# Kernel tuning notes

Measured on AMD Instinct MI355X. Metric: run time of the kernel, lower is better.

Reference implementation:

```python
import jax, jax.numpy as jnp
import numpy as np

ALPHA = 0.2  # LeakyReLU negative slope
MASK_VAL = -9e15


def setup_inputs() -> dict:
    key = jax.random.key(0)
    k1, k2, k3, k4 = jax.random.split(key, 4)
    B, N, F_IN = 4, 2048, 256
    H, HD = 8, 32  # out_features = H*HD = 256
    x = jax.random.normal(k1, (B, N, F_IN), dtype=jnp.float32)
    adj = jax.random.randint(k2, (B, N, N), 0, 2, dtype=jnp.int32)
    W = jax.random.normal(k3, (H, F_IN, HD), dtype=jnp.float32) * (1.0 / np.sqrt(F_IN))
    a = jax.random.normal(k4, (H, 2 * HD, 1), dtype=jnp.float32) * 0.1
    return {"x": x, "adj": adj, "W": W, "a": a}


def reference(x, adj, W, a):
    # x: (B,N,F), W: (H,F,D), a: (H,2D,1)
    B, N, _ = x.shape
    H, _, D = W.shape
    Wh = jnp.einsum('bnf,hfd->bhnd', x, W)  # (B,H,N,D)
    # Split additive attention vector: cat([Wh_i, Wh_j]) @ a == Wh_i@a1 + Wh_j@a2
    a1 = a[:, :D, 0]   # (H,D)
    a2 = a[:, D:, 0]   # (H,D)
    s1 = jnp.einsum('bhnd,hd->bhn', Wh, a1)  # source scores
    s2 = jnp.einsum('bhnd,hd->bhn', Wh, a2)  # target scores
    e = jax.nn.leaky_relu(s1[:, :, :, None] + s2[:, :, None, :], negative_slope=ALPHA)  # (B,H,N,N)
    e = jnp.where(adj[:, None, :, :] == 0, MASK_VAL, e)
    attention = jax.nn.softmax(e, axis=-1)  # dropout skipped (eval mode)
    h = jnp.einsum('bhij,bhjd->bhid', attention, Wh)  # (B,H,N,D)
    h = jnp.transpose(h, (0, 2, 1, 3)).reshape(B, N, H * D)
    return jax.nn.elu(h)
```

## Files before the change

kernel.cpp:

```cpp
#include <hip/hip_runtime.h>
#include <hip/hip_bf16.h>

#define ALPHA 0.2f

typedef __attribute__((ext_vector_type(8))) short short8;
typedef __attribute__((ext_vector_type(4))) short s4;
typedef __attribute__((ext_vector_type(8))) _Float16 h8;
typedef __attribute__((ext_vector_type(2))) _Float16 h2v;
typedef __attribute__((ext_vector_type(4))) float f32x4;
typedef __attribute__((ext_vector_type(2))) short sh2;

static constexpr int B = 4, N = 2048, F = 256, H = 8, D = 32;
static constexpr int SZ_X = B * N * F, SZ_ADJ = B * N * N, SZ_W = H * F * D, SZ_A = H * 2 * D;
static const float C1 = 1.4426950408889634f;
static const float C2 = ALPHA * 1.4426950408889634f;


__device__ __forceinline__ unsigned rne16(unsigned u) {
    return u + 0x7fffu + ((u >> 16) & 1u);
}
__device__ __forceinline__ unsigned pk_rne(float a, float b) {
    return __builtin_amdgcn_perm(rne16(__float_as_uint(b)),
                                 rne16(__float_as_uint(a)), 0x07060302u);
}
__device__ __forceinline__ unsigned h2mul(unsigned a, unsigned b) {
    h2v r = __builtin_bit_cast(h2v, a) * __builtin_bit_cast(h2v, b);
    return __builtin_bit_cast(unsigned, r);
}
__device__ __forceinline__ unsigned h2max(unsigned a, unsigned b) {
    h2v r = __builtin_elementwise_max(__builtin_bit_cast(h2v, a),
                                      __builtin_bit_cast(h2v, b));
    return __builtin_bit_cast(unsigned, r);
}
__device__ __forceinline__ unsigned dup16f(float x) {
    unsigned short w = __builtin_bit_cast(unsigned short, (_Float16)x);
    return (unsigned)w | ((unsigned)w << 16);
}
__device__ __forceinline__ unsigned bits2mask(unsigned mk, unsigned mulc) {
    unsigned w = (mk & 3u) * mulc;
    sh2 s = __builtin_bit_cast(sh2, w);
    s = s >> 15;
    return __builtin_bit_cast(unsigned, s);
}

__global__ void k0_prep(const float* __restrict__ Wp, const float* __restrict__ ap,
                        unsigned short* __restrict__ WT2, float* __restrict__ AF) {
    int bid = blockIdx.x;
    int h = bid >> 5, d = bid & 31;
    int f = threadIdx.x;
    unsigned short v = (unsigned short)(rne16(__float_as_uint(Wp[(h * F + f) * D + d])) >> 16);
    WT2[(size_t)(f >> 5) * 8192 + (h * 32 + d) * 32 + (f & 31)] = v;
    if (d == 0 && f < 64) AF[h * 64 + f] = ap[h * 64 + f];
}

__global__ __launch_bounds__(256) void k2_fused(const float* __restrict__ x,
                                                const unsigned short* __restrict__ WT2,
                                                const float* __restrict__ AF,
                                                unsigned short* __restrict__ WHT,
                                                float* __restrict__ S1,
                                                _Float16* __restrict__ UH,
                                                _Float16* __restrict__ VH,
                                                const int* __restrict__ adj,
                                                unsigned long long* __restrict__ bm) {
    __shared__ unsigned short XA[16 * 264];
    int bid = blockIdx.x;
    int rr = bid % 9;
    int grp = bid / 9;
    int t = threadIdx.x;

    if (rr != 8) {
        int wid = (grp * 8 + rr) * 4 + (t >> 6);
        int lane = t & 63;
        size_t base = (size_t)wid * 16;
        const int* ap2 = adj + base * 64 + lane;
        int v[16];
#pragma unroll
        for (int s = 0; s < 16; s++) v[s] = ap2[(size_t)s * 64];
        unsigned long long m[16];
#pragma unroll
        for (int s = 0; s < 16; s++) m[s] = __ballot(v[s] != 0);
        if (lane == 0) {
#pragma unroll
            for (int s = 0; s < 16; s++) bm[base + s] = m[s];
        }
        return;
    }

    int b = grp >> 7;
    int n0 = (grp & 127) * 16;
    int wave = t >> 6, lane = t & 63;
    int lm = lane & 15, lq = lane >> 4;

#pragma unroll
    for (int q = 0; q < 4; q++) {
        int idx = q * 256 + t;
        int row = idx >> 6, c16 = idx & 63;
        f32x4 v = *(const f32x4*)(x + (size_t)(b * N + n0 + row) * F + c16 * 4);
        unsigned* dst = (unsigned*)&XA[row * 264 + c16 * 4];
        dst[0] = pk_rne(v[0], v[1]);
        dst[1] = pk_rne(v[2], v[3]);
    }
    __syncthreads();

    f32x4 acc[4] = {};
#pragma unroll
    for (int kc = 0; kc < 8; kc++) {
        short8 afr = *(const short8*)&XA[lm * 264 + kc * 32 + lq * 8];
#pragma unroll
        for (int c = 0; c < 4; c++) {
            int hd = wave * 64 + c * 16 + lm;
            short8 bfr = *(const short8*)(WT2 + (size_t)kc * 8192 + hd * 32 + lq * 8);
            acc[c] = __builtin_amdgcn_mfma_f32_16x16x32_bf16(afr, bfr, acc[c], 0, 0, 0);
        }
    }

#pragma unroll
    for (int c = 0; c < 4; c++) {
        int hd = wave * 64 + c * 16 + lm;
        unsigned short w0 = __builtin_bit_cast(unsigned short, (_Float16)acc[c][0]);
        unsigned short w1 = __builtin_bit_cast(unsigned short, (_Float16)acc[c][1]);
        unsigned short w2 = __builtin_bit_cast(unsigned short, (_Float16)acc[c][2]);
        unsigned short w3 = __builtin_bit_cast(unsigned short, (_Float16)acc[c][3]);
        uint2 pk;
        pk.x = (unsigned)w0 | ((unsigned)w1 << 16);
        pk.y = (unsigned)w2 | ((unsigned)w3 << 16);
        *(uint2*)&WHT[((size_t)b * 256 + hd) * 2048 + n0 + lq * 4] = pk;
    }
#pragma unroll
    for (int cp = 0; cp < 2; cp++) {
        int h = wave * 2 + cp;
        float a1l = AF[h * 64 + lm],      a1h = AF[h * 64 + 16 + lm];
        float a2l = AF[h * 64 + 32 + lm], a2h = AF[h * 64 + 48 + lm];
#pragma unroll
        for (int r = 0; r < 4; r++) {
            float s1p = acc[cp * 2][r] * a1l + acc[cp * 2 + 1][r] * a1h;
            float s2p = acc[cp * 2][r] * a2l + acc[cp * 2 + 1][r] * a2h;
#pragma unroll
            for (int off = 1; off <= 8; off <<= 1) {
                s1p += __shfl_xor(s1p, off);
                s2p += __shfl_xor(s2p, off);
            }
            if (lm == 0) {
                int bh = b * 8 + h, n = n0 + lq * 4 + r;
                S1[(size_t)bh * 2048 + n] = s1p;
                UH[(size_t)bh * 2048 + n] = (_Float16)exp2f(C1 * s2p);
                VH[(size_t)bh * 2048 + n] = (_Float16)exp2f(C2 * s2p);
            }
        }
    }
}

__global__ __launch_bounds__(256) void k3_attn(
    const unsigned* __restrict__ bm32,
    const unsigned short* __restrict__ WHT,
    const float* __restrict__ S1,
    const _Float16* __restrict__ UH, const _Float16* __restrict__ VH,
    float* __restrict__ out) {
    __shared__ unsigned LM[4][32 * 66];
    __shared__ unsigned short LW[2][32 * 140];

    int bid = blockIdx.x;
    int bh = (bid & 7) + ((bid >> 7) << 3);
    int isup = (bid >> 3) & 15;
    int b = bh >> 3, h = bh & 7;
    int i0 = isup * 128;
    int t = threadIdx.x;
    int wave = t >> 6, lane = t & 63;
    int irow = lane & 15, quad = lane >> 4;
    int iw = i0 + wave * 32;

    {
        unsigned* lmp = LM[wave];
        const unsigned* src = bm32 + ((size_t)(b * N + iw)) * 64;
#pragma unroll 4
        for (int r = 0; r < 32; r++)
            lmp[r * 66 + lane] = src[(size_t)r * 64 + lane];
    }

    const unsigned short* wsrc = WHT + ((size_t)b * 256 + h * 32) * 2048;
    int srow = t >> 3, sseg = (t & 7) * 16;

    {
        const unsigned short* g = wsrc + (size_t)srow * 2048 + sseg;
        union { short8 v; s4 q[2]; } a, c;
        a.v = *(const short8*)(g);
        c.v = *(const short8*)(g + 8);
        unsigned short* d = &LW[0][srow * 140 + sseg];
        *(s4*)(d) = a.q[0]; *(s4*)(d + 4) = a.q[1];
        *(s4*)(d + 8) = c.q[0]; *(s4*)(d + 12) = c.q[1];
    }

    float s1A = S1[(size_t)bh * 2048 + iw + irow];
    float s1B = S1[(size_t)bh * 2048 + iw + 16 + irow];
    unsigned ci2A = dup16f(exp2f((C2 - C1) * s1A));
    unsigned ci2B = dup16f(exp2f((C2 - C1) * s1B));
    const _Float16* up = UH + (size_t)bh * 2048;
    const _Float16* vp = VH + (size_t)bh * 2048;

    union { h8 v; unsigned u[4]; } ones;
    ones.u[0] = ones.u[1] = ones.u[2] = ones.u[3] = 0x3C003C00u;

    const unsigned MUL = 0x40008000u;

    f32x4 aA0 = {0,0,0,0}, aA1 = {0,0,0,0}, aAL = {0,0,0,0};
    f32x4 aB0 = {0,0,0,0}, aB1 = {0,0,0,0}, aBL = {0,0,0,0};
    __syncthreads();

    for (int cc = 0; cc < 16; cc++) {
        union { short8 v; s4 q[2]; } pa, pc;
        if (cc < 15) {
            const unsigned short* g = wsrc + (size_t)srow * 2048 + (cc + 1) * 128 + sseg;
            pa.v = *(const short8*)(g);
            pc.v = *(const short8*)(g + 8);
        }
        const unsigned short* lwp = LW[cc & 1];
        const unsigned* lmw = LM[wave];
#pragma unroll
        for (int ks = 0; ks < 4; ks++) {
            int jl = ks * 32 + quad * 8;
            int jg = cc * 128 + jl;
            uint4 uw = *(const uint4*)(up + jg);
            uint4 vw = *(const uint4*)(vp + jg);
            unsigned mkA = lmw[irow * 66 + cc * 4 + ks] >> (quad * 8);
            unsigned mkB = lmw[(16 + irow) * 66 + cc * 4 + ks] >> (quad * 8);
            unsigned mA0 = bits2mask(mkA,      MUL);
            unsigned mA1 = bits2mask(mkA >> 2, MUL);
            unsigned mA2 = bits2mask(mkA >> 4, MUL);
            unsigned mA3 = bits2mask(mkA >> 6, MUL);
            unsigned mB0 = bits2mask(mkB,      MUL);
            unsigned mB1 = bits2mask(mkB >> 2, MUL);
            unsigned mB2 = bits2mask(mkB >> 4, MUL);
            unsigned mB3 = bits2mask(mkB >> 6, MUL);
            union { h8 v; unsigned u[4]; } afA, afB;
            afA.u[0] = h2max(uw.x, h2mul(ci2A, vw.x)) & mA0;
            afA.u[1] = h2max(uw.y, h2mul(ci2A, vw.y)) & mA1;
            afA.u[2] = h2max(uw.z, h2mul(ci2A, vw.z)) & mA2;
            afA.u[3] = h2max(uw.w, h2mul(ci2A, vw.w)) & mA3;
            afB.u[0] = h2max(uw.x, h2mul(ci2B, vw.x)) & mB0;
            afB.u[1] = h2max(uw.y, h2mul(ci2B, vw.y)) & mB1;
            afB.u[2] = h2max(uw.z, h2mul(ci2B, vw.z)) & mB2;
            afB.u[3] = h2max(uw.w, h2mul(ci2B, vw.w)) & mB3;
            union { short8 v; s4 q[2]; } bf0, bf1;
            bf0.q[0] = *(const s4*)&lwp[irow * 140 + jl];
            bf0.q[1] = *(const s4*)&lwp[irow * 140 + jl + 4];
            bf1.q[0] = *(const s4*)&lwp[(16 + irow) * 140 + jl];
            bf1.q[1] = *(const s4*)&lwp[(16 + irow) * 140 + jl + 4];
            h8 b0 = __builtin_bit_cast(h8, bf0.v);
            h8 b1 = __builtin_bit_cast(h8, bf1.v);
            aA0 = __builtin_amdgcn_mfma_f32_16x16x32_f16(afA.v, b0, aA0, 0, 0, 0);
            aA1 = __builtin_amdgcn_mfma_f32_16x16x32_f16(afA.v, b1, aA1, 0, 0, 0);
            aAL = __builtin_amdgcn_mfma_f32_16x16x32_f16(afA.v, ones.v, aAL, 0, 0, 0);
            aB0 = __builtin_amdgcn_mfma_f32_16x16x32_f16(afB.v, b0, aB0, 0, 0, 0);
            aB1 = __builtin_amdgcn_mfma_f32_16x16x32_f16(afB.v, b1, aB1, 0, 0, 0);
            aBL = __builtin_amdgcn_mfma_f32_16x16x32_f16(afB.v, ones.v, aBL, 0, 0, 0);
        }
        if (cc < 15) {
            unsigned short* d = &LW[(cc + 1) & 1][srow * 140 + sseg];
            *(s4*)(d) = pa.q[0]; *(s4*)(d + 4) = pa.q[1];
            *(s4*)(d + 8) = pc.q[0]; *(s4*)(d + 12) = pc.q[1];
        }
        __syncthreads();
    }

#pragma unroll
    for (int r = 0; r < 4; r++) {
        float lA = aAL[r], lB = aBL[r];
        float rA = 1.0f / (lA > 0.f ? lA : 1.f);
        float rB = 1.0f / (lB > 0.f ? lB : 1.f);
        float vA0 = aA0[r] * rA, vA1 = aA1[r] * rA;
        float vB0 = aB0[r] * rB, vB1 = aB1[r] * rB;
        vA0 = vA0 > 0.f ? vA0 : __expf(vA0) - 1.f;
        vA1 = vA1 > 0.f ? vA1 : __expf(vA1) - 1.f;
        vB0 = vB0 > 0.f ? vB0 : __expf(vB0) - 1.f;
        vB1 = vB1 > 0.f ? vB1 : __expf(vB1) - 1.f;
        int iA = iw + quad * 4 + r, iB = iA + 16;
        size_t rbA = (size_t)(b * N + iA) * 256 + h * 32;
        size_t rbB = (size_t)(b * N + iB) * 256 + h * 32;
        out[rbA + irow] = vA0;
        out[rbA + 16 + irow] = vA1;
        out[rbB + irow] = vB0;
        out[rbB + 16 + irow] = vB1;
    }
}

extern "C" void kernel_launch(void* const* d_in, const int* in_sizes, int n_in,
                              void* d_out, int out_size, void* d_ws, size_t ws_size,
                              hipStream_t stream) {
    const void *xP = nullptr, *adjP = nullptr, *WP = nullptr, *aP = nullptr;
    for (int i = 0; i < n_in; i++) {
        switch (in_sizes[i]) {
            case SZ_X:   xP = d_in[i]; break;
            case SZ_ADJ: adjP = d_in[i]; break;
            case SZ_W:   WP = d_in[i]; break;
            case SZ_A:   aP = d_in[i]; break;
            default: break;
        }
    }
    if (!xP || !adjP || !WP || !aP) { xP = d_in[0]; adjP = d_in[1]; WP = d_in[2]; aP = d_in[3]; }
    float* out = (float*)d_out;

    char* ws = (char*)d_ws;
    unsigned short* WT2 = (unsigned short*)(ws);
    float* AF  = (float*)(ws + 131072);
    float* S1  = (float*)(ws + 133120);
    _Float16* UH = (_Float16*)(ws + 395264);
    _Float16* VH = (_Float16*)(ws + 526336);
    unsigned short* WHT = (unsigned short*)(ws + 657408);
    unsigned long long* BM = (unsigned long long*)(ws + 4851712);

    k0_prep<<<256, 256, 0, stream>>>((const float*)WP, (const float*)aP, WT2, AF);
    k2_fused<<<4608, 256, 0, stream>>>((const float*)xP, WT2, AF, WHT, S1, UH, VH,
                                       (const int*)adjP, BM);
    k3_attn<<<512, 256, 0, stream>>>((const unsigned*)BM, WHT, S1, UH, VH, out);
}
```

Measured before the change: 144.1 us.

## Double adj-packing work per wave, prefetch W fragments, process two chunks per sync

In the fused projection kernel, each mask-packing wave now handles 32 adjacency rows instead of 16, so the grid shrinks from 4608 to 2560 blocks while keeping one projection block per group. The projection GEMM register-prefetches the next W fragments ahead of the MFMAs, and the kernel gets a launch_bounds occupancy hint. The attention kernel moves to a 4-slot LDS ring and handles two 128-column chunks per barrier, halving the __syncthreads count. The cost is more registers and LDS, which could lower occupancy.

```diff
diff --git a/kernel.cpp b/kernel.cpp
--- a/kernel.cpp
+++ b/kernel.cpp
@@ -53,35 +53,42 @@
     if (d == 0 && f < 64) AF[h * 64 + f] = ap[h * 64 + f];
 }
 
-__global__ __launch_bounds__(256) void k2_fused(const float* __restrict__ x,
-                                                const unsigned short* __restrict__ WT2,
-                                                const float* __restrict__ AF,
-                                                unsigned short* __restrict__ WHT,
-                                                float* __restrict__ S1,
-                                                _Float16* __restrict__ UH,
-                                                _Float16* __restrict__ VH,
-                                                const int* __restrict__ adj,
-                                                unsigned long long* __restrict__ bm) {
+__global__ __launch_bounds__(256, 4) void k2_fused(const float* __restrict__ x,
+                                                   const unsigned short* __restrict__ WT2,
+                                                   const float* __restrict__ AF,
+                                                   unsigned short* __restrict__ WHT,
+                                                   float* __restrict__ S1,
+                                                   _Float16* __restrict__ UH,
+                                                   _Float16* __restrict__ VH,
+                                                   const int* __restrict__ adj,
+                                                   unsigned long long* __restrict__ bm) {
     __shared__ unsigned short XA[16 * 264];
     int bid = blockIdx.x;
-    int rr = bid % 9;
-    int grp = bid / 9;
+    int rr = bid % 5;
+    int grp = bid / 5;
     int t = threadIdx.x;
 
-    if (rr != 8) {
-        int wid = (grp * 8 + rr) * 4 + (t >> 6);
+    if (rr != 4) {
+        int wid = (grp * 4 + rr) * 4 + (t >> 6);
         int lane = t & 63;
-        size_t base = (size_t)wid * 16;
+        size_t base = (size_t)wid * 32;
         const int* ap2 = adj + base * 64 + lane;
-        int v[16];
-#pragma unroll
-        for (int s = 0; s < 16; s++) v[s] = ap2[(size_t)s * 64];
-        unsigned long long m[16];
-#pragma unroll
-        for (int s = 0; s < 16; s++) m[s] = __ballot(v[s] != 0);
+        int v0[16], v1[16];
+#pragma unroll
+        for (int s = 0; s < 16; s++) v0[s] = ap2[(size_t)s * 64];
+#pragma unroll
+        for (int s = 0; s < 16; s++) v1[s] = ap2[(size_t)(16 + s) * 64];
+        unsigned long long m0[16];
+#pragma unroll
+        for (int s = 0; s < 16; s++) m0[s] = __ballot(v0[s] != 0);
+        unsigned long long m1[16];
+#pragma unroll
+        for (int s = 0; s < 16; s++) m1[s] = __ballot(v1[s] != 0);
         if (lane == 0) {
 #pragma unroll
-            for (int s = 0; s < 16; s++) bm[base + s] = m[s];
+            for (int s = 0; s < 16; s++) bm[base + s] = m0[s];
+#pragma unroll
+            for (int s = 0; s < 16; s++) bm[base + 16 + s] = m1[s];
         }
         return;
     }
@@ -100,18 +107,28 @@
         dst[0] = pk_rne(v[0], v[1]);
         dst[1] = pk_rne(v[2], v[3]);
     }
+
+    short8 bcur[4], bnext[4];
+#pragma unroll
+    for (int c = 0; c < 4; c++)
+        bcur[c] = *(const short8*)(WT2 + (size_t)(wave * 64 + c * 16 + lm) * 32 + lq * 8);
     __syncthreads();
 
     f32x4 acc[4] = {};
 #pragma unroll
     for (int kc = 0; kc < 8; kc++) {
+        if (kc < 7) {
+#pragma unroll
+            for (int c = 0; c < 4; c++)
+                bnext[c] = *(const short8*)(WT2 + (size_t)(kc + 1) * 8192 +
+                                            (wave * 64 + c * 16 + lm) * 32 + lq * 8);
+        }
         short8 afr = *(const short8*)&XA[lm * 264 + kc * 32 + lq * 8];
 #pragma unroll
-        for (int c = 0; c < 4; c++) {
-            int hd = wave * 64 + c * 16 + lm;
-            short8 bfr = *(const short8*)(WT2 + (size_t)kc * 8192 + hd * 32 + lq * 8);
-            acc[c] = __builtin_amdgcn_mfma_f32_16x16x32_bf16(afr, bfr, acc[c], 0, 0, 0);
-        }
+        for (int c = 0; c < 4; c++)
+            acc[c] = __builtin_amdgcn_mfma_f32_16x16x32_bf16(afr, bcur[c], acc[c], 0, 0, 0);
+#pragma unroll
+        for (int c = 0; c < 4; c++) bcur[c] = bnext[c];
     }
 
 #pragma unroll
@@ -157,7 +174,7 @@
     const _Float16* __restrict__ UH, const _Float16* __restrict__ VH,
     float* __restrict__ out) {
     __shared__ unsigned LM[4][32 * 66];
-    __shared__ unsigned short LW[2][32 * 140];
+    __shared__ unsigned short LW[4][32 * 140];
 
     int bid = blockIdx.x;
     int bh = (bid & 7) + ((bid >> 7) << 3);
@@ -172,7 +189,7 @@
     {
         unsigned* lmp = LM[wave];
         const unsigned* src = bm32 + ((size_t)(b * N + iw)) * 64;
-#pragma unroll 4
+#pragma unroll
         for (int r = 0; r < 32; r++)
             lmp[r * 66 + lane] = src[(size_t)r * 64 + lane];
     }
@@ -181,13 +198,18 @@
     int srow = t >> 3, sseg = (t & 7) * 16;
 
     {
-        const unsigned short* g = wsrc + (size_t)srow * 2048 + sseg;
-        union { short8 v; s4 q[2]; } a, c;
-        a.v = *(const short8*)(g);
-        c.v = *(const short8*)(g + 8);
-        unsigned short* d = &LW[0][srow * 140 + sseg];
-        *(s4*)(d) = a.q[0]; *(s4*)(d + 4) = a.q[1];
-        *(s4*)(d + 8) = c.q[0]; *(s4*)(d + 12) = c.q[1];
+        const unsigned short* g0 = wsrc + (size_t)srow * 2048 + sseg;
+        union { short8 v; s4 q[2]; } a0, c0, a1, c1;
+        a0.v = *(const short8*)(g0);
+        c0.v = *(const short8*)(g0 + 8);
+        a1.v = *(const short8*)(g0 + 128);
+        c1.v = *(const short8*)(g0 + 136);
+        unsigned short* d0 = &LW[0][srow * 140 + sseg];
+        *(s4*)(d0) = a0.q[0]; *(s4*)(d0 + 4) = a0.q[1];
+        *(s4*)(d0 + 8) = c0.q[0]; *(s4*)(d0 + 12) = c0.q[1];
+        unsigned short* d1 = &LW[1][srow * 140 + sseg];
+        *(s4*)(d1) = a1.q[0]; *(s4*)(d1 + 4) = a1.q[1];
+        *(s4*)(d1 + 8) = c1.q[0]; *(s4*)(d1 + 12) = c1.q[1];
     }
 
     float s1A = S1[(size_t)bh * 2048 + iw + irow];
@@ -206,58 +228,67 @@
     f32x4 aB0 = {0,0,0,0}, aB1 = {0,0,0,0}, aBL = {0,0,0,0};
     __syncthreads();
 
-    for (int cc = 0; cc < 16; cc++) {
-        union { short8 v; s4 q[2]; } pa, pc;
-        if (cc < 15) {
-            const unsigned short* g = wsrc + (size_t)srow * 2048 + (cc + 1) * 128 + sseg;
-            pa.v = *(const short8*)(g);
-            pc.v = *(const short8*)(g + 8);
-        }
-        const unsigned short* lwp = LW[cc & 1];
+    for (int g = 0; g < 8; g++) {
+        union { short8 v; s4 q[2]; } pa0, pc0, pa1, pc1;
+        if (g < 7) {
+            const unsigned short* g0 = wsrc + (size_t)srow * 2048 + (2 * g + 2) * 128 + sseg;
+            pa0.v = *(const short8*)(g0);
+            pc0.v = *(const short8*)(g0 + 8);
+            pa1.v = *(const short8*)(g0 + 128);
+            pc1.v = *(const short8*)(g0 + 136);
+        }
         const unsigned* lmw = LM[wave];
 #pragma unroll
-        for (int ks = 0; ks < 4; ks++) {
-            int jl = ks * 32 + quad * 8;
-            int jg = cc * 128 + jl;
-            uint4 uw = *(const uint4*)(up + jg);
-            uint4 vw = *(const uint4*)(vp + jg);
-            unsigned mkA = lmw[irow * 66 + cc * 4 + ks] >> (quad * 8);
-            unsigned mkB = lmw[(16 + irow) * 66 + cc * 4 + ks] >> (quad * 8);
-            unsigned mA0 = bits2mask(mkA,      MUL);
-            unsigned mA1 = bits2mask(mkA >> 2, MUL);
-            unsigned mA2 = bits2mask(mkA >> 4, MUL);
-            unsigned mA3 = bits2mask(mkA >> 6, MUL);
-            unsigned mB0 = bits2mask(mkB,      MUL);
-            unsigned mB1 = bits2mask(mkB >> 2, MUL);
-            unsigned mB2 = bits2mask(mkB >> 4, MUL);
-            unsigned mB3 = bits2mask(mkB >> 6, MUL);
-            union { h8 v; unsigned u[4]; } afA, afB;
-            afA.u[0] = h2max(uw.x, h2mul(ci2A, vw.x)) & mA0;
-            afA.u[1] = h2max(uw.y, h2mul(ci2A, vw.y)) & mA1;
-            afA.u[2] = h2max(uw.z, h2mul(ci2A, vw.z)) & mA2;
-            afA.u[3] = h2max(uw.w, h2mul(ci2A, vw.w)) & mA3;
-            afB.u[0] = h2max(uw.x, h2mul(ci2B, vw.x)) & mB0;
-            afB.u[1] = h2max(uw.y, h2mul(ci2B, vw.y)) & mB1;
-            afB.u[2] = h2max(uw.z, h2mul(ci2B, vw.z)) & mB2;
-            afB.u[3] = h2max(uw.w, h2mul(ci2B, vw.w)) & mB3;
-            union { short8 v; s4 q[2]; } bf0, bf1;
-            bf0.q[0] = *(const s4*)&lwp[irow * 140 + jl];
-            bf0.q[1] = *(const s4*)&lwp[irow * 140 + jl + 4];
-            bf1.q[0] = *(const s4*)&lwp[(16 + irow) * 140 + jl];
-            bf1.q[1] = *(const s4*)&lwp[(16 + irow) * 140 + jl + 4];
-            h8 b0 = __builtin_bit_cast(h8, bf0.v);
-            h8 b1 = __builtin_bit_cast(h8, bf1.v);
-            aA0 = __builtin_amdgcn_mfma_f32_16x16x32_f16(afA.v, b0, aA0, 0, 0, 0);
-            aA1 = __builtin_amdgcn_mfma_f32_16x16x32_f16(afA.v, b1, aA1, 0, 0, 0);
-            aAL = __builtin_amdgcn_mfma_f32_16x16x32_f16(afA.v, ones.v, aAL, 0, 0, 0);
-            aB0 = __builtin_amdgcn_mfma_f32_16x16x32_f16(afB.v, b0, aB0, 0, 0, 0);
-            aB1 = __builtin_amdgcn_mfma_f32_16x16x32_f16(afB.v, b1, aB1, 0, 0, 0);
-            aBL = __builtin_amdgcn_mfma_f32_16x16x32_f16(afB.v, ones.v, aBL, 0, 0, 0);
-        }
-        if (cc < 15) {
-            unsigned short* d = &LW[(cc + 1) & 1][srow * 140 + sseg];
-            *(s4*)(d) = pa.q[0]; *(s4*)(d + 4) = pa.q[1];
-            *(s4*)(d + 8) = pc.q[0]; *(s4*)(d + 12) = pc.q[1];
+        for (int ci = 0; ci < 2; ci++) {
+            int cc = 2 * g + ci;
+            const unsigned short* lwp = LW[cc & 3];
+#pragma unroll
+            for (int ks = 0; ks < 4; ks++) {
+                int jl = ks * 32 + quad * 8;
+                int jg = cc * 128 + jl;
+                uint4 uw = *(const uint4*)(up + jg);
+                uint4 vw = *(const uint4*)(vp + jg);
+                unsigned mkA = lmw[irow * 66 + cc * 4 + ks] >> (quad * 8);
+                unsigned mkB = lmw[(16 + irow) * 66 + cc * 4 + ks] >> (quad * 8);
+                unsigned mA0 = bits2mask(mkA,      MUL);
+                unsigned mA1 = bits2mask(mkA >> 2, MUL);
+                unsigned mA2 = bits2mask(mkA >> 4, MUL);
+                unsigned mA3 = bits2mask(mkA >> 6, MUL);
+                unsigned mB0 = bits2mask(mkB,      MUL);
+                unsigned mB1 = bits2mask(mkB >> 2, MUL);
+                unsigned mB2 = bits2mask(mkB >> 4, MUL);
+                unsigned mB3 = bits2mask(mkB >> 6, MUL);
+                union { h8 v; unsigned u[4]; } afA, afB;
+                afA.u[0] = h2max(uw.x, h2mul(ci2A, vw.x)) & mA0;
+                afA.u[1] = h2max(uw.y, h2mul(ci2A, vw.y)) & mA1;
+                afA.u[2] = h2max(uw.z, h2mul(ci2A, vw.z)) & mA2;
+                afA.u[3] = h2max(uw.w, h2mul(ci2A, vw.w)) & mA3;
+                afB.u[0] = h2max(uw.x, h2mul(ci2B, vw.x)) & mB0;
+                afB.u[1] = h2max(uw.y, h2mul(ci2B, vw.y)) & mB1;
+                afB.u[2] = h2max(uw.z, h2mul(ci2B, vw.z)) & mB2;
+                afB.u[3] = h2max(uw.w, h2mul(ci2B, vw.w)) & mB3;
+                union { short8 v; s4 q[2]; } bf0, bf1;
+                bf0.q[0] = *(const s4*)&lwp[irow * 140 + jl];
+                bf0.q[1] = *(const s4*)&lwp[irow * 140 + jl + 4];
+                bf1.q[0] = *(const s4*)&lwp[(16 + irow) * 140 + jl];
+                bf1.q[1] = *(const s4*)&lwp[(16 + irow) * 140 + jl + 4];
+                h8 b0 = __builtin_bit_cast(h8, bf0.v);
+                h8 b1 = __builtin_bit_cast(h8, bf1.v);
+                aA0 = __builtin_amdgcn_mfma_f32_16x16x32_f16(afA.v, b0, aA0, 0, 0, 0);
+                aA1 = __builtin_amdgcn_mfma_f32_16x16x32_f16(afA.v, b1, aA1, 0, 0, 0);
+                aAL = __builtin_amdgcn_mfma_f32_16x16x32_f16(afA.v, ones.v, aAL, 0, 0, 0);
+                aB0 = __builtin_amdgcn_mfma_f32_16x16x32_f16(afB.v, b0, aB0, 0, 0, 0);
+                aB1 = __builtin_amdgcn_mfma_f32_16x16x32_f16(afB.v, b1, aB1, 0, 0, 0);
+                aBL = __builtin_amdgcn_mfma_f32_16x16x32_f16(afB.v, ones.v, aBL, 0, 0, 0);
+            }
+        }
+        if (g < 7) {
+            unsigned short* d0 = &LW[(2 * g + 2) & 3][srow * 140 + sseg];
+            *(s4*)(d0) = pa0.q[0]; *(s4*)(d0 + 4) = pa0.q[1];
+            *(s4*)(d0 + 8) = pc0.q[0]; *(s4*)(d0 + 12) = pc0.q[1];
+            unsigned short* d1 = &LW[(2 * g + 3) & 3][srow * 140 + sseg];
+            *(s4*)(d1) = pa1.q[0]; *(s4*)(d1 + 4) = pa1.q[1];
+            *(s4*)(d1 + 8) = pc1.q[0]; *(s4*)(d1 + 12) = pc1.q[1];
         }
         __syncthreads();
     }
@@ -309,7 +340,7 @@
     unsigned long long* BM = (unsigned long long*)(ws + 4851712);
 
     k0_prep<<<256, 256, 0, stream>>>((const float*)WP, (const float*)aP, WT2, AF);
-    k2_fused<<<4608, 256, 0, stream>>>((const float*)xP, WT2, AF, WHT, S1, UH, VH,
+    k2_fused<<<2560, 256, 0, stream>>>((const float*)xP, WT2, AF, WHT, S1, UH, VH,
                                        (const int*)adjP, BM);
     k3_attn<<<512, 256, 0, stream>>>((const unsigned*)BM, WHT, S1, UH, VH, out);
 }
```

New measurement: 141.6 us. About the same (-1.7%).
